# Performance work log

Measured on AMD Instinct MI355X. Metric: run time of the kernel, lower is better.

## Reference

```python
import jax, jax.numpy as jnp
import numpy as np
import math

D_MODEL = 1024
NUM_HEADS = 16
HEAD_DIM = D_MODEL // NUM_HEADS  # 64
PLANE_DIM = HEAD_DIM // 2        # 32
ROPE_THETA = 10000.0
ROPE_PERIOD = 1024.0
ROPE_SCALE = 2.0 * math.pi / ROPE_PERIOD


def _inv_freq():
    # 1 / theta^(arange(0, plane_dim, 2)/plane_dim)  -> [plane_dim//2] = [16]
    return 1.0 / ROPE_THETA ** (jnp.arange(0, PLANE_DIM, 2, dtype=jnp.float32) / PLANE_DIM)


def _rotate_pairs(x, sin, cos):
    # x: [B,H,N,P], sin/cos: [B,1,N,P//2]
    x0 = x[..., 0::2]
    x1 = x[..., 1::2]
    y0 = x0 * cos - x1 * sin
    y1 = x0 * sin + x1 * cos
    return jnp.stack([y0, y1], axis=-1).reshape(x.shape)


def _apply_rope_2d(x, pos_2d, inv_freq):
    # x: [B,H,N,D], pos_2d: [B,N,2]
    ang_x = pos_2d[..., 0] * ROPE_SCALE  # [B,N]
    ang_y = pos_2d[..., 1] * ROPE_SCALE
    fx = ang_x[..., None] * inv_freq     # [B,N,P//2]
    fy = ang_y[..., None] * inv_freq
    sin_x, cos_x = jnp.sin(fx)[:, None], jnp.cos(fx)[:, None]  # [B,1,N,P//2]
    sin_y, cos_y = jnp.sin(fy)[:, None], jnp.cos(fy)[:, None]
    xp, yp = x[..., :PLANE_DIM], x[..., PLANE_DIM:]
    xp = _rotate_pairs(xp, sin_x, cos_x)
    yp = _rotate_pairs(yp, sin_y, cos_y)
    return jnp.concatenate([xp, yp], axis=-1)


def setup_inputs() -> dict:
    key = jax.random.key(0)
    ks = jax.random.split(key, 12)
    B, N, d = 2, 2048, D_MODEL
    s = 1.0 / math.sqrt(d)
    return {
        "x": jax.random.normal(ks[0], (B, N, d), jnp.float32),
        "q_positions": jax.random.uniform(ks[1], (B, N, 2), jnp.float32) * ROPE_PERIOD,
        "kv_positions": jax.random.uniform(ks[2], (B, N, 2), jnp.float32) * ROPE_PERIOD,
        "Wq": jax.random.normal(ks[3], (d, d), jnp.float32) * s,
        "bq": jnp.zeros((d,), jnp.float32),
        "Wk": jax.random.normal(ks[4], (d, d), jnp.float32) * s,
        "bk": jnp.zeros((d,), jnp.float32),
        "Wv": jax.random.normal(ks[5], (d, d), jnp.float32) * s,
        "bv": jnp.zeros((d,), jnp.float32),
        "Wo": jax.random.normal(ks[6], (d, d), jnp.float32) * s,
        "bo": jnp.zeros((d,), jnp.float32),
    }


def reference(x, q_positions, kv_positions, Wq, bq, Wk, bk, Wv, bv, Wo, bo):
    B, Nq, _ = x.shape
    H, D = NUM_HEADS, HEAD_DIM
    inv_freq = _inv_freq()
    # fused-style QKV projections (torch Linear: x @ W.T + b)
    q = (jnp.einsum('bnd,od->bno', x, Wq) + bq).reshape(B, Nq, H, D).transpose(0, 2, 1, 3)
    k = (jnp.einsum('bnd,od->bno', x, Wk) + bk).reshape(B, Nq, H, D).transpose(0, 2, 1, 3)
    v = (jnp.einsum('bnd,od->bno', x, Wv) + bv).reshape(B, Nq, H, D).transpose(0, 2, 1, 3)
    q = _apply_rope_2d(q, q_positions, inv_freq)
    k = _apply_rope_2d(k, kv_positions, inv_freq)
    logits = jnp.einsum('bhqd,bhkd->bhqk', q, k) / math.sqrt(D)
    attn = jax.nn.softmax(logits, axis=-1)
    out = jnp.einsum('bhqk,bhkd->bhqd', attn, v)
    out = out.transpose(0, 2, 1, 3).reshape(B, Nq, D_MODEL)
    return jnp.einsum('bnd,od->bno', out, Wo) + bo
```

## Files before the change

kernel.cpp:

```cpp
#include <hip/hip_runtime.h>
#include <math.h>

#define SEQ   2048
#define DM    1024
#define NTOK  4096
#define HEADS 16
#define HDIM  64
#define ROPE_SCALE 0.006135923151542565f
#define L2_10000   13.287712379549449f

typedef __attribute__((ext_vector_type(8))) short bf16x8;
typedef __attribute__((ext_vector_type(4))) float f32x4;

__device__ __forceinline__ unsigned short f2bf(float f) {
    unsigned int u = __float_as_uint(f);
    return (unsigned short)((u + 0x7FFFu + ((u >> 16) & 1u)) >> 16);
}
__device__ __forceinline__ float bf2f(unsigned short h) {
    return __uint_as_float(((unsigned int)h) << 16);
}

__device__ __forceinline__ void split8(const float* __restrict__ src, bf16x8& h, bf16x8& l) {
    float4 f0 = ((const float4*)src)[0];
    float4 f1 = ((const float4*)src)[1];
    float fv[8] = {f0.x,f0.y,f0.z,f0.w,f1.x,f1.y,f1.z,f1.w};
    #pragma unroll
    for (int j = 0; j < 8; ++j) {
        unsigned short hb = f2bf(fv[j]);
        h[j] = (short)hb;
        l[j] = (short)f2bf(fv[j] - bf2f(hb));
    }
}

__device__ __forceinline__ void gload16(const void* g, void* l) {
    __builtin_amdgcn_global_load_lds(
        (const __attribute__((address_space(1))) unsigned int*)g,
        (__attribute__((address_space(3))) unsigned int*)l, 16, 0, 0);
}

__global__ __launch_bounds__(256) void pack_swz(
    const float* __restrict__ src, unsigned short* __restrict__ dst)
{
    const int idx = blockIdx.x*256 + threadIdx.x;
    const int e = idx * 8;
    const int r = e >> 10, k0 = e & 1023;
    bf16x8 h, l;
    split8(src + (size_t)r*DM + k0, h, l);
    const int mt = r >> 7, rl = r & 127;
    const int kt = k0 >> 5, kl = k0 & 31;
    char* tb = (char*)(dst + ((size_t)(mt*32 + kt))*8192);
    const int sw = (rl & 7) << 4;
    *(bf16x8*)(tb + ((rl*128 + kl*2) ^ sw))      = h;
    *(bf16x8*)(tb + ((rl*128 + 64 + kl*2) ^ sw)) = l;
}

__global__ __launch_bounds__(256) void pack_swz3(
    const float* __restrict__ Wq, const float* __restrict__ Wk,
    const float* __restrict__ Wv, unsigned short* __restrict__ dst)
{
    const int idx = blockIdx.x*256 + threadIdx.x;
    const int e = idx * 8;
    const int r = e >> 10, k0 = e & 1023;
    const int proj = r >> 10;
    const float* W = proj==0 ? Wq : (proj==1 ? Wk : Wv);
    bf16x8 h, l;
    split8(W + (size_t)(r & 1023)*DM + k0, h, l);
    const int mt = r >> 7, rl = r & 127;
    const int kt = k0 >> 5, kl = k0 & 31;
    char* tb = (char*)(dst + ((size_t)(mt*32 + kt))*8192);
    const int sw = (rl & 7) << 4;
    *(bf16x8*)(tb + ((rl*128 + kl*2) ^ sw))      = h;
    *(bf16x8*)(tb + ((rl*128 + 64 + kl*2) ^ sw)) = l;
}

__global__ __launch_bounds__(256) void gemm_mfma(
    const unsigned short* __restrict__ Ap, const unsigned short* __restrict__ Bp,
    const int mode,
    const float* __restrict__ bq, const float* __restrict__ bk,
    const float* __restrict__ bv,
    const float* __restrict__ qpos, const float* __restrict__ kpos,
    float* __restrict__ qo, float* __restrict__ ko, float* __restrict__ vo,
    const float* __restrict__ bo, float* __restrict__ outp)
{
    __shared__ __align__(16) unsigned short Ab[2][8192];
    __shared__ __align__(16) unsigned short Bb[2][8192];

    const int tid = threadIdx.x, lane = tid & 63, wv = tid >> 6;
    const int col = lane & 15, grp = lane >> 4;
    const int wr = wv >> 1, wc = wv & 1;
    const int mt = blockIdx.y, nt = blockIdx.x;

    f32x4 acc[4][4];
    #pragma unroll
    for (int mf=0; mf<4; ++mf)
        #pragma unroll
        for (int nf=0; nf<4; ++nf)
            acc[mf][nf] = (f32x4)0.f;

    auto stage = [&](int buf, int kt) {
        const char* ga = (const char*)(Ap + ((size_t)(mt*32 + kt))*8192);
        const char* gb = (const char*)(Bp + ((size_t)(nt*32 + kt))*8192);
        char* la = (char*)&Ab[buf][0];
        char* lb = (char*)&Bb[buf][0];
        #pragma unroll
        for (int rep = 0; rep < 4; ++rep) {
            const int o = wv*4096 + rep*1024;
            gload16(ga + o + lane*16, la + o);
            gload16(gb + o + lane*16, lb + o);
        }
    };

    stage(0, 0);
    int cur = 0;
    for (int kt = 0; kt < 32; ++kt) {
        __syncthreads();
        if (kt < 31) stage(cur ^ 1, kt + 1);
        const char* A = (const char*)&Ab[cur][0];
        const char* B = (const char*)&Bb[cur][0];
        bf16x8 ah[4], al[4], bh[4], bl[4];
        #pragma unroll
        for (int mf = 0; mf < 4; ++mf) {
            const int rl = wr*64 + mf*16 + col;
            const int base = rl*128 + grp*16;
            const int sw = (rl & 7) << 4;
            ah[mf] = *(const bf16x8*)(A + (base ^ sw));
            al[mf] = *(const bf16x8*)(A + ((base + 64) ^ sw));
        }
        #pragma unroll
        for (int nf = 0; nf < 4; ++nf) {
            const int rl = wc*64 + nf*16 + col;
            const int base = rl*128 + grp*16;
            const int sw = (rl & 7) << 4;
            bh[nf] = *(const bf16x8*)(B + (base ^ sw));
            bl[nf] = *(const bf16x8*)(B + ((base + 64) ^ sw));
        }
        #pragma unroll
        for (int mf = 0; mf < 4; ++mf)
            #pragma unroll
            for (int nf = 0; nf < 4; ++nf) {
                acc[mf][nf] = __builtin_amdgcn_mfma_f32_16x16x32_bf16(ah[mf], bh[nf], acc[mf][nf], 0,0,0);
                acc[mf][nf] = __builtin_amdgcn_mfma_f32_16x16x32_bf16(ah[mf], bl[nf], acc[mf][nf], 0,0,0);
                acc[mf][nf] = __builtin_amdgcn_mfma_f32_16x16x32_bf16(al[mf], bh[nf], acc[mf][nf], 0,0,0);
            }
        cur ^= 1;
    }

    const int m0 = mt*128, n0 = nt*128;
    if (mode == 1) {
        #pragma unroll
        for (int nf = 0; nf < 4; ++nf) {
            const int n = n0 + wc*64 + nf*16 + col;
            const float bn = bo[n];
            #pragma unroll
            for (int mf = 0; mf < 4; ++mf)
                #pragma unroll
                for (int i = 0; i < 4; ++i) {
                    const int tok = m0 + wr*64 + mf*16 + grp*4 + i;
                    outp[(size_t)tok*DM + n] = acc[mf][nf][i] + bn;
                }
        }
    } else {
        const int proj = n0 >> 10;
        const float* bb = proj==0 ? bq : (proj==1 ? bk : bv);
        float* op       = proj==0 ? qo : (proj==1 ? ko : vo);
        const float* pp = proj==0 ? qpos : kpos;
        #pragma unroll
        for (int nf = 0; nf < 4; ++nf) {
            const int n  = n0 + wc*64 + nf*16 + col;
            const int nn = n & 1023;
            const int h  = nn >> 6, dd = nn & 63;
            const float bn = bb[nn];
            if (proj == 2) {
                #pragma unroll
                for (int mf = 0; mf < 4; ++mf)
                    #pragma unroll
                    for (int i = 0; i < 4; ++i) {
                        const int tok = m0 + wr*64 + mf*16 + grp*4 + i;
                        const int b = tok >> 11, sq = tok & 2047;
                        op[(((size_t)(b*HEADS + h))*SEQ + sq)*HDIM + dd] = acc[mf][nf][i] + bn;
                    }
            } else {
                const int plane = dd >> 5;
                const float e = (float)(dd & 30) * (1.0f/32.0f);
                const float invf = exp2f(-L2_10000 * e);
                #pragma unroll
                for (int mf = 0; mf < 4; ++mf)
                    #pragma unroll
                    for (int i = 0; i < 4; ++i) {
                        const int tok = m0 + wr*64 + mf*16 + grp*4 + i;
                        const int b = tok >> 11, sq = tok & 2047;
                        const float pv = pp[((size_t)(b*SEQ + sq))*2 + plane];
                        const float ang = pv * ROPE_SCALE * invf;
                        float s, c;
                        sincosf(ang, &s, &c);
                        const float val = acc[mf][nf][i] + bn;
                        const float prt = __shfl_xor(val, 1);
                        const float res = (dd & 1) ? (prt*s + val*c) : (val*c - prt*s);
                        op[(((size_t)(b*HEADS + h))*SEQ + sq)*HDIM + dd] = res;
                    }
            }
        }
    }
}

#define KB 32

__global__ __launch_bounds__(256) void attn_mfma(
    const float* __restrict__ q, const float* __restrict__ k,
    const float* __restrict__ v, float* __restrict__ ao)
{
    const int bh  = blockIdx.y;
    const int qb0 = blockIdx.x * 128;
    const int tid = threadIdx.x;
    const int lane = tid & 63;
    const int wv   = tid >> 6;
    const int col  = lane & 15;
    const int grp  = lane >> 4;

    __shared__ __align__(16) unsigned short Khi[KB][72];
    __shared__ __align__(16) unsigned short Klo[KB][72];
    __shared__ __align__(16) unsigned short Vthi[HDIM][40];
    __shared__ __align__(16) unsigned short Vtlo[HDIM][40];
    __shared__ __align__(16) unsigned short Pb[4][32][40];

    const float* kbase = k + (size_t)bh*SEQ*HDIM;
    const float* vbase = v + (size_t)bh*SEQ*HDIM;

    bf16x8 qhi[2][2], qlo[2][2];
    #pragma unroll
    for (int mf = 0; mf < 2; ++mf)
        #pragma unroll
        for (int ks = 0; ks < 2; ++ks) {
            const float* p = q + ((size_t)bh*SEQ + qb0 + wv*32 + mf*16 + col)*HDIM
                               + ks*32 + grp*8;
            split8(p, qhi[mf][ks], qlo[mf][ks]);
        }

    f32x4 o[2][4];
    #pragma unroll
    for (int mf=0; mf<2; ++mf)
        #pragma unroll
        for (int nf=0; nf<4; ++nf)
            o[mf][nf] = (f32x4)0.f;
    float mrun[2][4], lrun[2][4];
    #pragma unroll
    for (int mf=0; mf<2; ++mf)
        #pragma unroll
        for (int r=0; r<4; ++r) { mrun[mf][r] = -INFINITY; lrun[mf][r] = 0.f; }

    for (int kt = 0; kt < SEQ; kt += KB) {
        __syncthreads();
        {
            const int row = tid >> 3, c0 = (tid & 7) * 8;
            bf16x8 h, l;
            split8(kbase + (size_t)(kt + row)*HDIM + c0, h, l);
            *(bf16x8*)&Khi[row][c0] = h;
            *(bf16x8*)&Klo[row][c0] = l;
        }
        {
            const int key = tid & 31, db = tid >> 5;
            const float* src = vbase + (size_t)(kt + key)*HDIM + db*8;
            float4 f0 = ((const float4*)src)[0];
            float4 f1 = ((const float4*)src)[1];
            float fv[8] = {f0.x,f0.y,f0.z,f0.w,f1.x,f1.y,f1.z,f1.w};
            #pragma unroll
            for (int j = 0; j < 8; ++j) {
                unsigned short hb = f2bf(fv[j]);
                Vthi[db*8+j][key] = hb;
                Vtlo[db*8+j][key] = f2bf(fv[j] - bf2f(hb));
            }
        }
        __syncthreads();

        f32x4 s[2][2];
        #pragma unroll
        for (int mf=0; mf<2; ++mf)
            #pragma unroll
            for (int nf=0; nf<2; ++nf)
                s[mf][nf] = (f32x4)0.f;
        #pragma unroll
        for (int ks = 0; ks < 2; ++ks) {
            bf16x8 kh[2], kl[2];
            #pragma unroll
            for (int nf = 0; nf < 2; ++nf) {
                kh[nf] = *(const bf16x8*)&Khi[nf*16 + col][ks*32 + grp*8];
                kl[nf] = *(const bf16x8*)&Klo[nf*16 + col][ks*32 + grp*8];
            }
            #pragma unroll
            for (int mf = 0; mf < 2; ++mf)
                #pragma unroll
                for (int nf = 0; nf < 2; ++nf) {
                    s[mf][nf] = __builtin_amdgcn_mfma_f32_16x16x32_bf16(qhi[mf][ks], kh[nf], s[mf][nf], 0,0,0);
                    s[mf][nf] = __builtin_amdgcn_mfma_f32_16x16x32_bf16(qlo[mf][ks], kh[nf], s[mf][nf], 0,0,0);
                    s[mf][nf] = __builtin_amdgcn_mfma_f32_16x16x32_bf16(qhi[mf][ks], kl[nf], s[mf][nf], 0,0,0);
                }
        }

        #pragma unroll
        for (int mf=0; mf<2; ++mf)
            #pragma unroll
            for (int nf=0; nf<2; ++nf)
                s[mf][nf] *= 0.125f;

        #pragma unroll
        for (int mf = 0; mf < 2; ++mf) {
            #pragma unroll
            for (int r = 0; r < 4; ++r) {
                float m2 = fmaxf(s[mf][0][r], s[mf][1][r]);
                m2 = fmaxf(m2, __shfl_xor(m2, 1, 16));
                m2 = fmaxf(m2, __shfl_xor(m2, 2, 16));
                m2 = fmaxf(m2, __shfl_xor(m2, 4, 16));
                m2 = fmaxf(m2, __shfl_xor(m2, 8, 16));
                const float mnew = fmaxf(mrun[mf][r], m2);
                const float corr = __expf(mrun[mf][r] - mnew);
                mrun[mf][r] = mnew;
                const float p0 = __expf(s[mf][0][r] - mnew);
                const float p1 = __expf(s[mf][1][r] - mnew);
                float ts = p0 + p1;
                ts += __shfl_xor(ts, 1, 16);
                ts += __shfl_xor(ts, 2, 16);
                ts += __shfl_xor(ts, 4, 16);
                ts += __shfl_xor(ts, 8, 16);
                lrun[mf][r] = lrun[mf][r]*corr + ts;
                #pragma unroll
                for (int nf=0; nf<4; ++nf) o[mf][nf][r] *= corr;
                Pb[wv][mf*16 + grp*4 + r][col]      = f2bf(p0);
                Pb[wv][mf*16 + grp*4 + r][16 + col] = f2bf(p1);
            }
        }

        bf16x8 pa[2];
        #pragma unroll
        for (int mf=0; mf<2; ++mf)
            pa[mf] = *(const bf16x8*)&Pb[wv][mf*16 + col][grp*8];
        #pragma unroll
        for (int nf = 0; nf < 4; ++nf) {
            bf16x8 vh = *(const bf16x8*)&Vthi[nf*16 + col][grp*8];
            bf16x8 vl = *(const bf16x8*)&Vtlo[nf*16 + col][grp*8];
            #pragma unroll
            for (int mf = 0; mf < 2; ++mf) {
                o[mf][nf] = __builtin_amdgcn_mfma_f32_16x16x32_bf16(pa[mf], vh, o[mf][nf], 0,0,0);
                o[mf][nf] = __builtin_amdgcn_mfma_f32_16x16x32_bf16(pa[mf], vl, o[mf][nf], 0,0,0);
            }
        }
    }

    const int b = bh >> 4, h = bh & 15;
    #pragma unroll
    for (int mf = 0; mf < 2; ++mf)
        #pragma unroll
        for (int r = 0; r < 4; ++r) {
            const float inv = 1.0f / lrun[mf][r];
            const int n = qb0 + wv*32 + mf*16 + grp*4 + r;
            float* orow = ao + (((size_t)b*SEQ + n)*HEADS + h)*HDIM;
            #pragma unroll
            for (int nf = 0; nf < 4; ++nf)
                orow[nf*16 + col] = o[mf][nf][r] * inv;
        }
}

extern "C" void kernel_launch(void* const* d_in, const int* in_sizes, int n_in,
                              void* d_out, int out_size, void* d_ws, size_t ws_size,
                              hipStream_t stream)
{
    const float* x    = (const float*)d_in[0];
    const float* qpos = (const float*)d_in[1];
    const float* kpos = (const float*)d_in[2];
    const float* Wq   = (const float*)d_in[3];
    const float* bq   = (const float*)d_in[4];
    const float* Wk   = (const float*)d_in[5];
    const float* bk   = (const float*)d_in[6];
    const float* Wv   = (const float*)d_in[7];
    const float* bv   = (const float*)d_in[8];
    const float* Wo   = (const float*)d_in[9];
    const float* bo   = (const float*)d_in[10];
    float* out = (float*)d_out;

    float* qw = (float*)d_ws;
    float* kw = qw + (size_t)NTOK*DM;
    float* vw = kw + (size_t)NTOK*DM;
    unsigned short* Xp    = (unsigned short*)(vw + (size_t)NTOK*DM);
    unsigned short* Wqkvp = Xp + (size_t)NTOK*DM*2;
    unsigned short* Wop   = Wqkvp + (size_t)3*DM*DM*2;

    pack_swz <<<2048, 256, 0, stream>>>(x, Xp);
    pack_swz3<<<1536, 256, 0, stream>>>(Wq, Wk, Wv, Wqkvp);
    pack_swz <<< 512, 256, 0, stream>>>(Wo, Wop);

    gemm_mfma<<<dim3(24, 32), 256, 0, stream>>>(
        Xp, Wqkvp, 0, bq, bk, bv, qpos, kpos, qw, kw, vw, nullptr, nullptr);

    attn_mfma<<<dim3(SEQ/128, 2*HEADS), 256, 0, stream>>>(qw, kw, vw, out);

    pack_swz <<<2048, 256, 0, stream>>>(out, Xp);

    gemm_mfma<<<dim3(8, 32), 256, 0, stream>>>(
        Xp, Wop, 1, nullptr, nullptr, nullptr, nullptr, nullptr,
        nullptr, nullptr, nullptr, bo, out);
}
```

Measured before the change: 657.5 us.

## Enlarge GEMM block tile to 256x256 with 512 threads and eight waves

The projection GEMMs now use a 256x256 output tile per block, with 8 waves arranged 2x4. Each wave computes a 128x64 sub-tile and reuses each loaded B fragment across 8 A fragments. This raises arithmetic intensity per LDS and global load and halves the packed-tile traffic per output element. The cost is far fewer blocks (192 for QKV, 64 for the output projection) on a device with many CUs, plus higher register and LDS pressure per block.

```diff
diff --git a/kernel.cpp b/kernel.cpp
--- a/kernel.cpp
+++ b/kernel.cpp
@@ -73,7 +73,7 @@
     *(bf16x8*)(tb + ((rl*128 + 64 + kl*2) ^ sw)) = l;
 }
 
-__global__ __launch_bounds__(256) void gemm_mfma(
+__global__ __launch_bounds__(512, 2) void gemm_mfma(
     const unsigned short* __restrict__ Ap, const unsigned short* __restrict__ Bp,
     const int mode,
     const float* __restrict__ bq, const float* __restrict__ bk,
@@ -82,31 +82,37 @@
     float* __restrict__ qo, float* __restrict__ ko, float* __restrict__ vo,
     const float* __restrict__ bo, float* __restrict__ outp)
 {
-    __shared__ __align__(16) unsigned short Ab[2][8192];
-    __shared__ __align__(16) unsigned short Bb[2][8192];
+    __shared__ __align__(16) unsigned short Ab[2][16384];
+    __shared__ __align__(16) unsigned short Bb[2][16384];
 
     const int tid = threadIdx.x, lane = tid & 63, wv = tid >> 6;
     const int col = lane & 15, grp = lane >> 4;
-    const int wr = wv >> 1, wc = wv & 1;
+    const int wr = wv >> 2, wc = wv & 3;
     const int mt = blockIdx.y, nt = blockIdx.x;
 
-    f32x4 acc[4][4];
-    #pragma unroll
-    for (int mf=0; mf<4; ++mf)
+    f32x4 acc[8][4];
+    #pragma unroll
+    for (int mf=0; mf<8; ++mf)
         #pragma unroll
         for (int nf=0; nf<4; ++nf)
             acc[mf][nf] = (f32x4)0.f;
 
     auto stage = [&](int buf, int kt) {
-        const char* ga = (const char*)(Ap + ((size_t)(mt*32 + kt))*8192);
-        const char* gb = (const char*)(Bp + ((size_t)(nt*32 + kt))*8192);
-        char* la = (char*)&Ab[buf][0];
-        char* lb = (char*)&Bb[buf][0];
-        #pragma unroll
-        for (int rep = 0; rep < 4; ++rep) {
-            const int o = wv*4096 + rep*1024;
-            gload16(ga + o + lane*16, la + o);
-            gload16(gb + o + lane*16, lb + o);
+        #pragma unroll
+        for (int rep = 0; rep < 8; ++rep) {
+            const int off = wv*8192 + rep*1024;
+            if (off < 32768) {
+                const int th = off >> 14, inner = off & 16383;
+                const char* g = (const char*)Ap
+                    + ((size_t)((mt*2 + th)*32 + kt))*16384 + inner;
+                gload16(g + lane*16, (char*)&Ab[buf][0] + off);
+            } else {
+                const int o2 = off - 32768;
+                const int th = o2 >> 14, inner = o2 & 16383;
+                const char* g = (const char*)Bp
+                    + ((size_t)((nt*2 + th)*32 + kt))*16384 + inner;
+                gload16(g + lane*16, (char*)&Bb[buf][0] + o2);
+            }
         }
     };
 
@@ -117,45 +123,47 @@
         if (kt < 31) stage(cur ^ 1, kt + 1);
         const char* A = (const char*)&Ab[cur][0];
         const char* B = (const char*)&Bb[cur][0];
-        bf16x8 ah[4], al[4], bh[4], bl[4];
-        #pragma unroll
-        for (int mf = 0; mf < 4; ++mf) {
-            const int rl = wr*64 + mf*16 + col;
-            const int base = rl*128 + grp*16;
-            const int sw = (rl & 7) << 4;
-            ah[mf] = *(const bf16x8*)(A + (base ^ sw));
-            al[mf] = *(const bf16x8*)(A + ((base + 64) ^ sw));
+        bf16x8 ah[8], al[8];
+        #pragma unroll
+        for (int mf = 0; mf < 8; ++mf) {
+            const int rl = wr*128 + mf*16 + col;
+            const int th = rl >> 7, r7 = rl & 127;
+            const int b0 = r7*128 + grp*16;
+            const int sw = (r7 & 7) << 4;
+            const char* base = A + th*16384;
+            ah[mf] = *(const bf16x8*)(base + (b0 ^ sw));
+            al[mf] = *(const bf16x8*)(base + ((b0 + 64) ^ sw));
         }
         #pragma unroll
         for (int nf = 0; nf < 4; ++nf) {
             const int rl = wc*64 + nf*16 + col;
-            const int base = rl*128 + grp*16;
-            const int sw = (rl & 7) << 4;
-            bh[nf] = *(const bf16x8*)(B + (base ^ sw));
-            bl[nf] = *(const bf16x8*)(B + ((base + 64) ^ sw));
-        }
-        #pragma unroll
-        for (int mf = 0; mf < 4; ++mf)
-            #pragma unroll
-            for (int nf = 0; nf < 4; ++nf) {
-                acc[mf][nf] = __builtin_amdgcn_mfma_f32_16x16x32_bf16(ah[mf], bh[nf], acc[mf][nf], 0,0,0);
-                acc[mf][nf] = __builtin_amdgcn_mfma_f32_16x16x32_bf16(ah[mf], bl[nf], acc[mf][nf], 0,0,0);
-                acc[mf][nf] = __builtin_amdgcn_mfma_f32_16x16x32_bf16(al[mf], bh[nf], acc[mf][nf], 0,0,0);
-            }
+            const int th = rl >> 7, r7 = rl & 127;
+            const int b0 = r7*128 + grp*16;
+            const int sw = (r7 & 7) << 4;
+            const char* base = B + th*16384;
+            bf16x8 bh  = *(const bf16x8*)(base + (b0 ^ sw));
+            bf16x8 blo = *(const bf16x8*)(base + ((b0 + 64) ^ sw));
+            #pragma unroll
+            for (int mf = 0; mf < 8; ++mf) {
+                acc[mf][nf] = __builtin_amdgcn_mfma_f32_16x16x32_bf16(ah[mf], bh,  acc[mf][nf], 0,0,0);
+                acc[mf][nf] = __builtin_amdgcn_mfma_f32_16x16x32_bf16(ah[mf], blo, acc[mf][nf], 0,0,0);
+                acc[mf][nf] = __builtin_amdgcn_mfma_f32_16x16x32_bf16(al[mf], bh,  acc[mf][nf], 0,0,0);
+            }
+        }
         cur ^= 1;
     }
 
-    const int m0 = mt*128, n0 = nt*128;
+    const int m0 = mt*256, n0 = nt*256;
     if (mode == 1) {
         #pragma unroll
         for (int nf = 0; nf < 4; ++nf) {
             const int n = n0 + wc*64 + nf*16 + col;
             const float bn = bo[n];
             #pragma unroll
-            for (int mf = 0; mf < 4; ++mf)
+            for (int mf = 0; mf < 8; ++mf)
                 #pragma unroll
                 for (int i = 0; i < 4; ++i) {
-                    const int tok = m0 + wr*64 + mf*16 + grp*4 + i;
+                    const int tok = m0 + wr*128 + mf*16 + grp*4 + i;
                     outp[(size_t)tok*DM + n] = acc[mf][nf][i] + bn;
                 }
         }
@@ -172,10 +180,10 @@
             const float bn = bb[nn];
             if (proj == 2) {
                 #pragma unroll
-                for (int mf = 0; mf < 4; ++mf)
+                for (int mf = 0; mf < 8; ++mf)
                     #pragma unroll
                     for (int i = 0; i < 4; ++i) {
-                        const int tok = m0 + wr*64 + mf*16 + grp*4 + i;
+                        const int tok = m0 + wr*128 + mf*16 + grp*4 + i;
                         const int b = tok >> 11, sq = tok & 2047;
                         op[(((size_t)(b*HEADS + h))*SEQ + sq)*HDIM + dd] = acc[mf][nf][i] + bn;
                     }
@@ -184,10 +192,10 @@
                 const float e = (float)(dd & 30) * (1.0f/32.0f);
                 const float invf = exp2f(-L2_10000 * e);
                 #pragma unroll
-                for (int mf = 0; mf < 4; ++mf)
+                for (int mf = 0; mf < 8; ++mf)
                     #pragma unroll
                     for (int i = 0; i < 4; ++i) {
-                        const int tok = m0 + wr*64 + mf*16 + grp*4 + i;
+                        const int tok = m0 + wr*128 + mf*16 + grp*4 + i;
                         const int b = tok >> 11, sq = tok & 2047;
                         const float pv = pp[((size_t)(b*SEQ + sq))*2 + plane];
                         const float ang = pv * ROPE_SCALE * invf;
@@ -387,14 +395,14 @@
     pack_swz3<<<1536, 256, 0, stream>>>(Wq, Wk, Wv, Wqkvp);
     pack_swz <<< 512, 256, 0, stream>>>(Wo, Wop);
 
-    gemm_mfma<<<dim3(24, 32), 256, 0, stream>>>(
+    gemm_mfma<<<dim3(12, 16), 512, 0, stream>>>(
         Xp, Wqkvp, 0, bq, bk, bv, qpos, kpos, qw, kw, vw, nullptr, nullptr);
 
     attn_mfma<<<dim3(SEQ/128, 2*HEADS), 256, 0, stream>>>(qw, kw, vw, out);
 
     pack_swz <<<2048, 256, 0, stream>>>(out, Xp);
 
-    gemm_mfma<<<dim3(8, 32), 256, 0, stream>>>(
+    gemm_mfma<<<dim3(4, 16), 512, 0, stream>>>(
         Xp, Wop, 1, nullptr, nullptr, nullptr, nullptr, nullptr,
         nullptr, nullptr, nullptr, bo, out);
 }
```

Result: slower. 877.3 us (+33.4%).

## Stage GEMM tiles through registers with a two-deep prefetch instead of direct-to-LDS loads

Applied to the files above, without the earlier changes.

The GEMM main loop no longer uses global_load_lds to copy tiles straight into shared memory. Tiles are now loaded into registers one k-step ahead and written to the LDS double buffer after the barrier, with the k-loop unrolled by two so each buffer has fixed registers. B fragments are also read per column inside the MFMA loop instead of all up front, which shortens fragment register lifetimes. The aim is better overlap of global loads with MFMA work, at the cost of more VGPRs for the staged tiles and extra ds_write instructions.

```diff
diff --git a/kernel.cpp b/kernel.cpp
--- a/kernel.cpp
+++ b/kernel.cpp
@@ -30,12 +30,6 @@
         h[j] = (short)hb;
         l[j] = (short)f2bf(fv[j] - bf2f(hb));
     }
-}
-
-__device__ __forceinline__ void gload16(const void* g, void* l) {
-    __builtin_amdgcn_global_load_lds(
-        (const __attribute__((address_space(1))) unsigned int*)g,
-        (__attribute__((address_space(3))) unsigned int*)l, 16, 0, 0);
 }
 
 __global__ __launch_bounds__(256) void pack_swz(
@@ -97,52 +91,64 @@
         for (int nf=0; nf<4; ++nf)
             acc[mf][nf] = (f32x4)0.f;
 
-    auto stage = [&](int buf, int kt) {
-        const char* ga = (const char*)(Ap + ((size_t)(mt*32 + kt))*8192);
-        const char* gb = (const char*)(Bp + ((size_t)(nt*32 + kt))*8192);
-        char* la = (char*)&Ab[buf][0];
-        char* lb = (char*)&Bb[buf][0];
-        #pragma unroll
-        for (int rep = 0; rep < 4; ++rep) {
-            const int o = wv*4096 + rep*1024;
-            gload16(ga + o + lane*16, la + o);
-            gload16(gb + o + lane*16, lb + o);
+    auto loadrefs = [&](int kt, float4* ra, float4* rb) {
+        const char* ga = (const char*)Ap + ((size_t)(mt*32 + kt))*16384;
+        const char* gb = (const char*)Bp + ((size_t)(nt*32 + kt))*16384;
+        #pragma unroll
+        for (int i = 0; i < 4; ++i) {
+            ra[i] = *(const float4*)(ga + tid*16 + i*4096);
+            rb[i] = *(const float4*)(gb + tid*16 + i*4096);
         }
     };
-
-    stage(0, 0);
-    int cur = 0;
-    for (int kt = 0; kt < 32; ++kt) {
-        __syncthreads();
-        if (kt < 31) stage(cur ^ 1, kt + 1);
-        const char* A = (const char*)&Ab[cur][0];
-        const char* B = (const char*)&Bb[cur][0];
-        bf16x8 ah[4], al[4], bh[4], bl[4];
+    auto dswrite = [&](int buf, const float4* ra, const float4* rb) {
+        #pragma unroll
+        for (int i = 0; i < 4; ++i) {
+            *(float4*)((char*)&Ab[buf][0] + tid*16 + i*4096) = ra[i];
+            *(float4*)((char*)&Bb[buf][0] + tid*16 + i*4096) = rb[i];
+        }
+    };
+    auto compute = [&](const unsigned short* As_, const unsigned short* Bs_) {
+        const char* A = (const char*)As_;
+        const char* B = (const char*)Bs_;
+        bf16x8 ah[4], al[4];
         #pragma unroll
         for (int mf = 0; mf < 4; ++mf) {
             const int rl = wr*64 + mf*16 + col;
-            const int base = rl*128 + grp*16;
+            const int b0 = rl*128 + grp*16;
             const int sw = (rl & 7) << 4;
-            ah[mf] = *(const bf16x8*)(A + (base ^ sw));
-            al[mf] = *(const bf16x8*)(A + ((base + 64) ^ sw));
+            ah[mf] = *(const bf16x8*)(A + (b0 ^ sw));
+            al[mf] = *(const bf16x8*)(A + ((b0 + 64) ^ sw));
         }
         #pragma unroll
         for (int nf = 0; nf < 4; ++nf) {
             const int rl = wc*64 + nf*16 + col;
-            const int base = rl*128 + grp*16;
+            const int b0 = rl*128 + grp*16;
             const int sw = (rl & 7) << 4;
-            bh[nf] = *(const bf16x8*)(B + (base ^ sw));
-            bl[nf] = *(const bf16x8*)(B + ((base + 64) ^ sw));
-        }
-        #pragma unroll
-        for (int mf = 0; mf < 4; ++mf)
-            #pragma unroll
-            for (int nf = 0; nf < 4; ++nf) {
-                acc[mf][nf] = __builtin_amdgcn_mfma_f32_16x16x32_bf16(ah[mf], bh[nf], acc[mf][nf], 0,0,0);
-                acc[mf][nf] = __builtin_amdgcn_mfma_f32_16x16x32_bf16(ah[mf], bl[nf], acc[mf][nf], 0,0,0);
-                acc[mf][nf] = __builtin_amdgcn_mfma_f32_16x16x32_bf16(al[mf], bh[nf], acc[mf][nf], 0,0,0);
-            }
-        cur ^= 1;
+            bf16x8 bh  = *(const bf16x8*)(B + (b0 ^ sw));
+            bf16x8 blo = *(const bf16x8*)(B + ((b0 + 64) ^ sw));
+            #pragma unroll
+            for (int mf = 0; mf < 4; ++mf) {
+                acc[mf][nf] = __builtin_amdgcn_mfma_f32_16x16x32_bf16(ah[mf], bh,  acc[mf][nf], 0,0,0);
+                acc[mf][nf] = __builtin_amdgcn_mfma_f32_16x16x32_bf16(ah[mf], blo, acc[mf][nf], 0,0,0);
+                acc[mf][nf] = __builtin_amdgcn_mfma_f32_16x16x32_bf16(al[mf], bh,  acc[mf][nf], 0,0,0);
+            }
+        }
+    };
+
+    float4 a0[4], b0[4], a1[4], b1[4];
+    loadrefs(0, a0, b0);
+    dswrite(0, a0, b0);
+    loadrefs(1, a1, b1);
+
+    for (int kt = 0; kt < 32; kt += 2) {
+        __syncthreads();
+        if (kt + 1 < 32) dswrite(1, a1, b1);
+        if (kt + 2 < 32) loadrefs(kt + 2, a0, b0);
+        compute(&Ab[0][0], &Bb[0][0]);
+        __syncthreads();
+        if (kt + 2 < 32) dswrite(0, a0, b0);
+        if (kt + 3 < 32) loadrefs(kt + 3, a1, b1);
+        compute(&Ab[1][0], &Bb[1][0]);
     }
 
     const int m0 = mt*128, n0 = nt*128;
```

After: 855.9 us. 1.3x slower.
